# Performance work log

Measured on AMD Instinct MI355X. Metric: run time of the kernel, lower is better.

The kernel has to match this reference:

```python
import jax, jax.numpy as jnp
import numpy as np

H = 16
D_MODEL = 1024
D_K = D_MODEL // H


def setup_inputs() -> dict:
    key = jax.random.key(0)
    ks = jax.random.split(key, 11)
    B, S = 2, 2048
    scale = 1.0 / np.sqrt(D_MODEL)
    inp = {
        "query": jax.random.normal(ks[0], (B, S, D_MODEL), dtype=jnp.float32),
        "key": jax.random.normal(ks[1], (B, S, D_MODEL), dtype=jnp.float32),
        "value": jax.random.normal(ks[2], (B, S, D_MODEL), dtype=jnp.float32),
        "Wq": jax.random.normal(ks[3], (D_MODEL, D_MODEL), dtype=jnp.float32) * scale,
        "bq": jnp.zeros((D_MODEL,), dtype=jnp.float32),
        "Wk": jax.random.normal(ks[4], (D_MODEL, D_MODEL), dtype=jnp.float32) * scale,
        "bk": jnp.zeros((D_MODEL,), dtype=jnp.float32),
        "Wv": jax.random.normal(ks[5], (D_MODEL, D_MODEL), dtype=jnp.float32) * scale,
        "bv": jnp.zeros((D_MODEL,), dtype=jnp.float32),
        "Wo": jax.random.normal(ks[6], (D_MODEL, D_MODEL), dtype=jnp.float32) * scale,
        "bo": jnp.zeros((D_MODEL,), dtype=jnp.float32),
    }
    return inp


def _mha(query, key, value, Wq, bq, Wk, bk, Wv, bv, Wo, bo):
    B, S, _ = query.shape
    # linear projections (torch nn.Linear: x @ W.T + b)
    q = query @ Wq.T + bq
    k = key @ Wk.T + bk
    v = value @ Wv.T + bv
    # split heads: [B, S, D] -> [B, H, S, d_k]
    q = q.reshape(B, S, H, D_K).transpose(0, 2, 1, 3)
    k = k.reshape(B, S, H, D_K).transpose(0, 2, 1, 3)
    v = v.reshape(B, S, H, D_K).transpose(0, 2, 1, 3)
    # scaled dot-product attention with manual stable softmax
    scores = jnp.einsum("bhqd,bhkd->bhqk", q, k) / jnp.sqrt(jnp.float32(D_K))
    stable = scores - jnp.max(scores, axis=-1, keepdims=True)
    e = jnp.exp(stable)
    attn = e / jnp.sum(e, axis=-1, keepdims=True)
    ctx = jnp.einsum("bhqk,bhkd->bhqd", attn, v)
    # merge heads and final projection
    ctx = ctx.transpose(0, 2, 1, 3).reshape(B, S, H * D_K)
    return ctx @ Wo.T + bo


def reference(query, key, value, Wq, bq, Wk, bk, Wv, bv, Wo, bo):
    return _mha(query, key, value, Wq, bq, Wk, bk, Wv, bv, Wo, bo)
```

## Files before the change

kernel.cpp:

```cpp
#include <hip/hip_runtime.h>


#define S_LEN 2048
#define BATCH 2
#define DM    1024
#define NH    16
#define DKH   64
#define BS    (BATCH * S_LEN)

typedef _Float16 f16x8 __attribute__((ext_vector_type(8)));
typedef _Float16 f16x4 __attribute__((ext_vector_type(4)));
typedef _Float16 f16x2 __attribute__((ext_vector_type(2)));
typedef __fp16   h16x2 __attribute__((ext_vector_type(2)));
typedef float    f32x4 __attribute__((ext_vector_type(4)));
typedef float    f32x16 __attribute__((ext_vector_type(16)));

__device__ __forceinline__ f16x2 pk_f16(float a, float b) {
  h16x2 r = __builtin_amdgcn_cvt_pkrtz(a, b);
  return __builtin_bit_cast(f16x2, r);
}

__device__ __forceinline__ void gld16(const void* g, void* l) {
  __builtin_amdgcn_global_load_lds(
      (const __attribute__((address_space(1))) void*)g,
      (__attribute__((address_space(3))) void*)l, 16, 0, 0);
}

__device__ __forceinline__ float fast_exp2(float x) {
#if __has_builtin(__builtin_amdgcn_exp2f)
  return __builtin_amdgcn_exp2f(x);
#else
  return exp2f(x);
#endif
}

__device__ __forceinline__ int swap23(int x) {
  return (x & ~12) | ((x & 4) << 1) | ((x & 8) >> 1);
}

__global__ __launch_bounds__(256) void cvt_all(
    const float* __restrict__ q, const float* __restrict__ k, const float* __restrict__ v,
    const float* __restrict__ wq, const float* __restrict__ wk,
    const float* __restrict__ wv, const float* __restrict__ wo,
    _Float16* __restrict__ xq, _Float16* __restrict__ xk, _Float16* __restrict__ xv,
    _Float16* __restrict__ w16)
{
  const int y = blockIdx.y;
  const float* src; _Float16* dst; int n;
  if (y == 0)      { src = q;  dst = xq; n = BS * DM; }
  else if (y == 1) { src = k;  dst = xk; n = BS * DM; }
  else if (y == 2) { src = v;  dst = xv; n = BS * DM; }
  else {
    src = (y == 3) ? wq : ((y == 4) ? wk : ((y == 5) ? wv : wo));
    dst = w16 + (size_t)(y - 3) * (DM * DM);
    n = DM * DM;
  }
  int i0 = (blockIdx.x * 256 + threadIdx.x) * 4;
  if (i0 < n) {
    float4 f = *(const float4*)(src + i0);
    f16x2 lo = pk_f16(f.x, f.y);
    f16x2 hi = pk_f16(f.z, f.w);
    f16x4 hh; hh[0] = lo[0]; hh[1] = lo[1]; hh[2] = hi[0]; hh[3] = hi[1];
    *(f16x4*)(dst + i0) = hh;
  }
}

template <typename OUT_T, bool VT>
__device__ __forceinline__ void gemm_core(
    const _Float16* __restrict__ A, const _Float16* __restrict__ W,
    const float* __restrict__ bias, OUT_T* __restrict__ out, float oscale)
{
  const int tid  = threadIdx.x;
  const int l    = tid & 63;
  const int wv   = tid >> 6;
  const int c    = l & 15, quad = l >> 4;
  const int m0   = blockIdx.y * 128, n0 = blockIdx.x * 128;
  const int wm   = wv & 1, wn = wv >> 1;
  __shared__ _Float16 sA[128 * 64];
  __shared__ _Float16 sB[128 * 64];

  const _Float16* gA[4]; const _Float16* gB[4];
#pragma unroll
  for (int p = 0; p < 4; ++p) {
    int s = tid + p * 256, r = s >> 3, g = (s & 7) ^ (r & 7);
    gA[p] = A + (size_t)(m0 + r) * DM + g * 8;
    gB[p] = W + (size_t)(n0 + r) * DM + g * 8;
  }
  const int cx = c & 7;

  f32x4 acc[4][4] = {};
  for (int k0 = 0; k0 < DM; k0 += 64) {
    __syncthreads();
#pragma unroll
    for (int p = 0; p < 4; ++p) {
      gld16(gA[p] + k0, sA + (tid + p * 256) * 8);
      gld16(gB[p] + k0, sB + (tid + p * 256) * 8);
    }
    __syncthreads();
#pragma unroll
    for (int ks = 0; ks < 2; ++ks) {
      f16x8 af[4], bf[4];
#pragma unroll
      for (int i = 0; i < 4; ++i)
        af[i] = *(const f16x8*)&sA[(wm * 64 + i * 16 + c) * 64 + ((ks * 4 + quad) ^ cx) * 8];
#pragma unroll
      for (int j = 0; j < 4; ++j)
        bf[j] = *(const f16x8*)&sB[(wn * 64 + j * 16 + c) * 64 + ((ks * 4 + quad) ^ cx) * 8];
#pragma unroll
      for (int i = 0; i < 4; ++i)
#pragma unroll
        for (int j = 0; j < 4; ++j)
          acc[i][j] = __builtin_amdgcn_mfma_f32_16x16x32_f16(af[i], bf[j], acc[i][j], 0, 0, 0);
    }
  }
  if constexpr (VT) {
#pragma unroll
    for (int j = 0; j < 4; ++j) {
      int col = n0 + wn * 64 + j * 16 + c;
      float bb = bias[col];
      int hh = col >> 6, dd = col & 63;
#pragma unroll
      for (int i = 0; i < 4; ++i) {
        int row = m0 + wm * 64 + i * 16 + quad * 4;
        int bb2 = row >> 11, ss = row & (S_LEN - 1);
        _Float16* dst = (_Float16*)out + ((size_t)(bb2 * NH + hh) * DKH + dd) * S_LEN + ss;
        f16x4 v4;
#pragma unroll
        for (int r = 0; r < 4; ++r) v4[r] = (_Float16)((acc[i][j][r] + bb) * oscale);
        *(f16x4*)dst = v4;
      }
    }
  } else {
#pragma unroll
    for (int j = 0; j < 4; ++j) {
      int col = n0 + wn * 64 + j * 16 + c;
      float bb = bias[col];
#pragma unroll
      for (int i = 0; i < 4; ++i) {
        int row = m0 + wm * 64 + i * 16 + quad * 4;
#pragma unroll
        for (int r = 0; r < 4; ++r) {
          float vv = (acc[i][j][r] + bb) * oscale;
          out[(size_t)(row + r) * DM + col] = (OUT_T)vv;
        }
      }
    }
  }
}

#define SC_Q (0.125f * 1.44269504088896340736f)

__global__ __launch_bounds__(256) void proj3(
    const _Float16* __restrict__ xq, const _Float16* __restrict__ xk,
    const _Float16* __restrict__ xv, const _Float16* __restrict__ w16,
    const float* __restrict__ bq, const float* __restrict__ bk, const float* __restrict__ bv,
    _Float16* __restrict__ Q, _Float16* __restrict__ K, _Float16* __restrict__ Vt)
{
  const int z = blockIdx.z;
  if (z == 2) {
    gemm_core<_Float16, true>(xv, w16 + (size_t)2 * DM * DM, bv, Vt, 1.0f);
  } else if (z == 0) {
    gemm_core<_Float16, false>(xq, w16, bq, Q, SC_Q);
  } else {
    gemm_core<_Float16, false>(xk, w16 + (size_t)DM * DM, bk, K, 1.0f);
  }
}

__global__ __launch_bounds__(256) void out_gemm(
    const _Float16* __restrict__ ctx, const _Float16* __restrict__ wo,
    const float* __restrict__ bo, float* __restrict__ out)
{
  gemm_core<float, false>(ctx, wo, bo, out, 1.0f);
}

__global__ __launch_bounds__(256, 4) void attn(
    const _Float16* __restrict__ Q, const _Float16* __restrict__ K,
    const _Float16* __restrict__ Vt, _Float16* __restrict__ ctx)
{
  const int tid = threadIdx.x;
  const int l   = tid & 63, wv = tid >> 6;
  const int lo5 = l & 31, hf = l >> 5;
  const int wq  = wv >> 1, wk = wv & 1;
  const int q0  = blockIdx.x * 64;
  const int bh  = blockIdx.y;
  const int b   = bh >> 4, hd = bh & 15;
  __shared__ _Float16 sK[2][64 * 64];
  __shared__ _Float16 sV[2][64 * 64];

  f16x8 qf[4];
  {
    const _Float16* Qg = Q + ((size_t)(b * S_LEN + q0 + wq * 32 + lo5)) * DM + hd * DKH + 8 * hf;
#pragma unroll
    for (int kc = 0; kc < 4; ++kc) qf[kc] = *(const f16x8*)(Qg + 16 * kc);
  }

  f32x16 o[2] = {};
  float l_part = 0.f;
  const f16x2 ones = {(_Float16)1.0f, (_Float16)1.0f};

  const _Float16* Kg0 = K + ((size_t)b * S_LEN) * DM + hd * DKH;
  const _Float16* Vg0 = Vt + ((size_t)bh * DKH) * S_LEN;

  const int sa = tid,       ra = sa >> 3, ba = (sa & 7) ^ (ra & 7);
  const int sb = tid + 256, rb = sb >> 3, bb = (sb & 7) ^ (rb & 7);
  const _Float16* gKa = Kg0 + (size_t)swap23(ra) * DM + ba * 8;
  const _Float16* gKb = Kg0 + (size_t)swap23(rb) * DM + bb * 8;
  const _Float16* gVa = Vg0 + (size_t)ra * S_LEN + ba * 8;
  const _Float16* gVb = Vg0 + (size_t)rb * S_LEN + bb * 8;
  const int rx = lo5 & 7;

#define STAGE(t, bf) do {                                   \
    const size_t k0s = (size_t)(t) * 64;                    \
    gld16(gKa + k0s * DM, sK[bf] + sa * 8);                 \
    gld16(gKb + k0s * DM, sK[bf] + sb * 8);                 \
    gld16(gVa + k0s,      sV[bf] + sa * 8);                 \
    gld16(gVb + k0s,      sV[bf] + sb * 8);                 \
  } while (0)

  STAGE(0, 0);
  asm volatile("s_waitcnt vmcnt(0)" ::: "memory");
  __builtin_amdgcn_s_barrier();

  const int NT = S_LEN / 64;
  for (int kt = 0; kt < NT; ++kt) {
    const int cur = kt & 1;
    if (kt + 1 < NT) STAGE(kt + 1, cur ^ 1);

    const _Float16* sKc = sK[cur];
    const _Float16* sVc = sV[cur];

    f32x16 sAcc = {};
    __builtin_amdgcn_s_setprio(1);
#pragma unroll
    for (int kc = 0; kc < 4; ++kc) {
      f16x8 kf = *(const f16x8*)&sKc[(32 * wk + lo5) * 64 + ((2 * kc + hf) ^ rx) * 8];
      sAcc = __builtin_amdgcn_mfma_f32_32x32x16_f16(kf, qf[kc], sAcc, 0, 0, 0);
    }
    __builtin_amdgcn_s_setprio(0);

    f16x8 pPv[2];
#pragma unroll
    for (int half = 0; half < 2; ++half)
#pragma unroll
      for (int j2 = 0; j2 < 4; ++j2) {
        float p0 = fast_exp2(sAcc[8 * half + 2 * j2]);
        float p1 = fast_exp2(sAcc[8 * half + 2 * j2 + 1]);
        f16x2 pk = pk_f16(p0, p1);
        pPv[half][2 * j2]     = pk[0];
        pPv[half][2 * j2 + 1] = pk[1];
        l_part = __builtin_amdgcn_fdot2(__builtin_bit_cast(h16x2, pk),
                                        __builtin_bit_cast(h16x2, ones), l_part, false);
      }

    __builtin_amdgcn_s_setprio(1);
#pragma unroll
    for (int db = 0; db < 2; ++db)
#pragma unroll
      for (int half = 0; half < 2; ++half) {
        const int kc2 = 2 * wk + half;
        f16x8 vf = *(const f16x8*)&sVc[(32 * db + lo5) * 64 + ((2 * kc2 + hf) ^ rx) * 8];
        o[db] = __builtin_amdgcn_mfma_f32_32x32x16_f16(pPv[half], vf, o[db], 0, 0, 0);
      }
    __builtin_amdgcn_s_setprio(0);

    if (kt + 1 < NT) {
      asm volatile("s_waitcnt vmcnt(0)" ::: "memory");
      __builtin_amdgcn_s_barrier();
    }
  }
#undef STAGE

  __syncthreads();

  l_part += __shfl_xor(l_part, 32);
  float* lbuf = (float*)&sK[0][0];
  float* obuf = (float*)&sV[0][0];
  if (hf == 0) lbuf[wv * 32 + lo5] = l_part;
  if (wk == 1) {
#pragma unroll
    for (int db = 0; db < 2; ++db)
#pragma unroll
      for (int r = 0; r < 16; ++r) {
        int qq = 8 * (r >> 2) + 4 * hf + (r & 3);
        obuf[(wq * 32 + qq) * 64 + 32 * db + lo5] = o[db][r];
      }
  }
  __syncthreads();

  if (wk == 0) {
    _Float16* Og = ctx + ((size_t)(b * S_LEN + q0 + wq * 32)) * DM + hd * DKH;
#pragma unroll
    for (int r = 0; r < 16; ++r) {
      int qq = 8 * (r >> 2) + 4 * hf + (r & 3);
      float inv = 1.0f / (lbuf[(2 * wq) * 32 + qq] + lbuf[(2 * wq + 1) * 32 + qq]);
#pragma unroll
      for (int db = 0; db < 2; ++db) {
        float val = o[db][r] + obuf[(wq * 32 + qq) * 64 + 32 * db + lo5];
        Og[(size_t)qq * DM + 32 * db + lo5] = (_Float16)(val * inv);
      }
    }
  }
}

extern "C" void kernel_launch(void* const* d_in, const int* in_sizes, int n_in,
                              void* d_out, int out_size, void* d_ws, size_t ws_size,
                              hipStream_t stream)
{
  (void)in_sizes; (void)n_in; (void)out_size; (void)ws_size;
  const float* q  = (const float*)d_in[0];
  const float* k  = (const float*)d_in[1];
  const float* v  = (const float*)d_in[2];
  const float* wq = (const float*)d_in[3];
  const float* bq = (const float*)d_in[4];
  const float* wk = (const float*)d_in[5];
  const float* bk = (const float*)d_in[6];
  const float* wv = (const float*)d_in[7];
  const float* bv = (const float*)d_in[8];
  const float* wo = (const float*)d_in[9];
  const float* bo = (const float*)d_in[10];

  char* ws = (char*)d_ws;
  _Float16* XQ  = (_Float16*)(ws);
  _Float16* XK  = (_Float16*)(ws + (8u  << 20));
  _Float16* XV  = (_Float16*)(ws + (16u << 20));
  _Float16* W16 = (_Float16*)(ws + (24u << 20));
  _Float16* Qp  = (_Float16*)(ws + (32u << 20));
  _Float16* Kp  = (_Float16*)(ws + (40u << 20));
  _Float16* VT  = (_Float16*)(ws + (48u << 20));
  _Float16* CTX = XQ;
  float* out = (float*)d_out;

  cvt_all<<<dim3(4096, 7), 256, 0, stream>>>(q, k, v, wq, wk, wv, wo, XQ, XK, XV, W16);
  proj3<<<dim3(8, 32, 3), 256, 0, stream>>>(XQ, XK, XV, W16, bq, bk, bv, Qp, Kp, VT);
  attn<<<dim3(32, 32), 256, 0, stream>>>(Qp, Kp, VT, CTX);
  out_gemm<<<dim3(8, 32), 256, 0, stream>>>(CTX, W16 + (size_t)3 * DM * DM, bo, out);
}
```

Before: 236.6 us.

## Process two 32-row query tiles per warp in attention to reuse K/V

The attention kernel now handles 128 query rows per block instead of 64, and each warp computes two query sub-tiles against the same K and V fragments loaded from shared memory. This halves the number of blocks and the global-to-LDS K/V traffic per query row, and raises the MFMA-to-LDS-read ratio. In exchange, register pressure roughly doubles (launch bounds lowered to 2 blocks per SM), there are fewer blocks in the grid (512), and the epilogue reduction is split into two passes with extra barriers.

```diff
diff --git a/kernel.cpp b/kernel.cpp
--- a/kernel.cpp
+++ b/kernel.cpp
@@ -173,7 +173,7 @@
   gemm_core<float, false>(ctx, wo, bo, out, 1.0f);
 }
 
-__global__ __launch_bounds__(256, 4) void attn(
+__global__ __launch_bounds__(256, 2) void attn(
     const _Float16* __restrict__ Q, const _Float16* __restrict__ K,
     const _Float16* __restrict__ Vt, _Float16* __restrict__ ctx)
 {
@@ -181,21 +181,23 @@
   const int l   = tid & 63, wv = tid >> 6;
   const int lo5 = l & 31, hf = l >> 5;
   const int wq  = wv >> 1, wk = wv & 1;
-  const int q0  = blockIdx.x * 64;
+  const int q0  = blockIdx.x * 128;
   const int bh  = blockIdx.y;
   const int b   = bh >> 4, hd = bh & 15;
   __shared__ _Float16 sK[2][64 * 64];
   __shared__ _Float16 sV[2][64 * 64];
 
-  f16x8 qf[4];
+  f16x8 qf0[4], qf1[4];
   {
-    const _Float16* Qg = Q + ((size_t)(b * S_LEN + q0 + wq * 32 + lo5)) * DM + hd * DKH + 8 * hf;
-#pragma unroll
-    for (int kc = 0; kc < 4; ++kc) qf[kc] = *(const f16x8*)(Qg + 16 * kc);
-  }
-
-  f32x16 o[2] = {};
-  float l_part = 0.f;
+    const _Float16* Qg0 = Q + ((size_t)(b * S_LEN + q0 + wq * 64 + lo5)) * DM + hd * DKH + 8 * hf;
+    const _Float16* Qg1 = Qg0 + (size_t)32 * DM;
+#pragma unroll
+    for (int kc = 0; kc < 4; ++kc) { qf0[kc] = *(const f16x8*)(Qg0 + 16 * kc);
+                                     qf1[kc] = *(const f16x8*)(Qg1 + 16 * kc); }
+  }
+
+  f32x16 o0[2] = {}, o1[2] = {};
+  float l0 = 0.f, l1 = 0.f;
   const f16x2 ones = {(_Float16)1.0f, (_Float16)1.0f};
 
   const _Float16* Kg0 = K + ((size_t)b * S_LEN) * DM + hd * DKH;
@@ -229,27 +231,35 @@
     const _Float16* sKc = sK[cur];
     const _Float16* sVc = sV[cur];
 
-    f32x16 sAcc = {};
+    f32x16 sA0 = {}, sA1 = {};
     __builtin_amdgcn_s_setprio(1);
 #pragma unroll
     for (int kc = 0; kc < 4; ++kc) {
       f16x8 kf = *(const f16x8*)&sKc[(32 * wk + lo5) * 64 + ((2 * kc + hf) ^ rx) * 8];
-      sAcc = __builtin_amdgcn_mfma_f32_32x32x16_f16(kf, qf[kc], sAcc, 0, 0, 0);
+      sA0 = __builtin_amdgcn_mfma_f32_32x32x16_f16(kf, qf0[kc], sA0, 0, 0, 0);
+      sA1 = __builtin_amdgcn_mfma_f32_32x32x16_f16(kf, qf1[kc], sA1, 0, 0, 0);
     }
     __builtin_amdgcn_s_setprio(0);
 
-    f16x8 pPv[2];
+    f16x8 p0[2], p1[2];
 #pragma unroll
     for (int half = 0; half < 2; ++half)
 #pragma unroll
       for (int j2 = 0; j2 < 4; ++j2) {
-        float p0 = fast_exp2(sAcc[8 * half + 2 * j2]);
-        float p1 = fast_exp2(sAcc[8 * half + 2 * j2 + 1]);
-        f16x2 pk = pk_f16(p0, p1);
-        pPv[half][2 * j2]     = pk[0];
-        pPv[half][2 * j2 + 1] = pk[1];
-        l_part = __builtin_amdgcn_fdot2(__builtin_bit_cast(h16x2, pk),
-                                        __builtin_bit_cast(h16x2, ones), l_part, false);
+        float a0 = fast_exp2(sA0[8 * half + 2 * j2]);
+        float a1 = fast_exp2(sA0[8 * half + 2 * j2 + 1]);
+        f16x2 pka = pk_f16(a0, a1);
+        p0[half][2 * j2]     = pka[0];
+        p0[half][2 * j2 + 1] = pka[1];
+        l0 = __builtin_amdgcn_fdot2(__builtin_bit_cast(h16x2, pka),
+                                    __builtin_bit_cast(h16x2, ones), l0, false);
+        float b0 = fast_exp2(sA1[8 * half + 2 * j2]);
+        float b1 = fast_exp2(sA1[8 * half + 2 * j2 + 1]);
+        f16x2 pkb = pk_f16(b0, b1);
+        p1[half][2 * j2]     = pkb[0];
+        p1[half][2 * j2 + 1] = pkb[1];
+        l1 = __builtin_amdgcn_fdot2(__builtin_bit_cast(h16x2, pkb),
+                                    __builtin_bit_cast(h16x2, ones), l1, false);
       }
 
     __builtin_amdgcn_s_setprio(1);
@@ -259,7 +269,8 @@
       for (int half = 0; half < 2; ++half) {
         const int kc2 = 2 * wk + half;
         f16x8 vf = *(const f16x8*)&sVc[(32 * db + lo5) * 64 + ((2 * kc2 + hf) ^ rx) * 8];
-        o[db] = __builtin_amdgcn_mfma_f32_32x32x16_f16(pPv[half], vf, o[db], 0, 0, 0);
+        o0[db] = __builtin_amdgcn_mfma_f32_32x32x16_f16(p0[half], vf, o0[db], 0, 0, 0);
+        o1[db] = __builtin_amdgcn_mfma_f32_32x32x16_f16(p1[half], vf, o1[db], 0, 0, 0);
       }
     __builtin_amdgcn_s_setprio(0);
 
@@ -272,33 +283,49 @@
 
   __syncthreads();
 
-  l_part += __shfl_xor(l_part, 32);
-  float* lbuf = (float*)&sK[0][0];
-  float* obuf = (float*)&sV[0][0];
-  if (hf == 0) lbuf[wv * 32 + lo5] = l_part;
-  if (wk == 1) {
-#pragma unroll
-    for (int db = 0; db < 2; ++db)
+  l0 += __shfl_xor(l0, 32);
+  l1 += __shfl_xor(l1, 32);
+  float* lbuf = (float*)&sV[0][0];
+  float* obuf = (float*)&sK[0][0];
+  if (hf == 0) {
+    lbuf[((wq * 2 + 0) * 2 + wk) * 32 + lo5] = l0;
+    lbuf[((wq * 2 + 1) * 2 + wk) * 32 + lo5] = l1;
+  }
+  __syncthreads();
+
+  float inv0[16], inv1[16];
+#pragma unroll
+  for (int r = 0; r < 16; ++r) {
+    int qq = 8 * (r >> 2) + 4 * hf + (r & 3);
+    inv0[r] = 1.0f / (lbuf[((wq * 2 + 0) * 2 + 0) * 32 + qq] +
+                      lbuf[((wq * 2 + 0) * 2 + 1) * 32 + qq]);
+    inv1[r] = 1.0f / (lbuf[((wq * 2 + 1) * 2 + 0) * 32 + qq] +
+                      lbuf[((wq * 2 + 1) * 2 + 1) * 32 + qq]);
+  }
+
+  _Float16* Og = ctx + ((size_t)(b * S_LEN + q0 + wq * 64)) * DM + hd * DKH;
+#pragma unroll
+  for (int db = 0; db < 2; ++db) {
+    if (wk == 1) {
 #pragma unroll
       for (int r = 0; r < 16; ++r) {
         int qq = 8 * (r >> 2) + 4 * hf + (r & 3);
-        obuf[(wq * 32 + qq) * 64 + 32 * db + lo5] = o[db][r];
-      }
-  }
-  __syncthreads();
-
-  if (wk == 0) {
-    _Float16* Og = ctx + ((size_t)(b * S_LEN + q0 + wq * 32)) * DM + hd * DKH;
-#pragma unroll
-    for (int r = 0; r < 16; ++r) {
-      int qq = 8 * (r >> 2) + 4 * hf + (r & 3);
-      float inv = 1.0f / (lbuf[(2 * wq) * 32 + qq] + lbuf[(2 * wq + 1) * 32 + qq]);
-#pragma unroll
-      for (int db = 0; db < 2; ++db) {
-        float val = o[db][r] + obuf[(wq * 32 + qq) * 64 + 32 * db + lo5];
-        Og[(size_t)qq * DM + 32 * db + lo5] = (_Float16)(val * inv);
-      }
-    }
+        obuf[((wq * 2 + 0) * 32 + qq) * 32 + lo5] = o0[db][r];
+        obuf[((wq * 2 + 1) * 32 + qq) * 32 + lo5] = o1[db][r];
+      }
+    }
+    __syncthreads();
+    if (wk == 0) {
+#pragma unroll
+      for (int r = 0; r < 16; ++r) {
+        int qq = 8 * (r >> 2) + 4 * hf + (r & 3);
+        float v0 = o0[db][r] + obuf[((wq * 2 + 0) * 32 + qq) * 32 + lo5];
+        float v1 = o1[db][r] + obuf[((wq * 2 + 1) * 32 + qq) * 32 + lo5];
+        Og[(size_t)qq * DM + 32 * db + lo5]        = (_Float16)(v0 * inv0[r]);
+        Og[(size_t)(32 + qq) * DM + 32 * db + lo5] = (_Float16)(v1 * inv1[r]);
+      }
+    }
+    __syncthreads();
   }
 }
 
@@ -332,6 +359,6 @@
 
   cvt_all<<<dim3(4096, 7), 256, 0, stream>>>(q, k, v, wq, wk, wv, wo, XQ, XK, XV, W16);
   proj3<<<dim3(8, 32, 3), 256, 0, stream>>>(XQ, XK, XV, W16, bq, bk, bv, Qp, Kp, VT);
-  attn<<<dim3(32, 32), 256, 0, stream>>>(Qp, Kp, VT, CTX);
+  attn<<<dim3(16, 32), 256, 0, stream>>>(Qp, Kp, VT, CTX);
   out_gemm<<<dim3(8, 32), 256, 0, stream>>>(CTX, W16 + (size_t)3 * DM * DM, bo, out);
 }
```

Result: no change. 233.4 us (-1.3%).
